# Performance work log

Hardware: AMD Instinct MI355X
Metric: run time of the kernel (lower is better)

Reference implementation:

```python
import jax, jax.numpy as jnp
import numpy as np

H = 51  # hidden size hardcoded in the module

def _lstm_cell(x, h, c, W_ih, W_hh, b_ih, b_hh):
    # PyTorch LSTMCell: gates ordered (i, f, g, o)
    z = x @ W_ih.T + h @ W_hh.T + b_ih + b_hh  # [B, 4H]
    i, f, g, o = jnp.split(z, 4, axis=-1)
    i = jax.nn.sigmoid(i)
    f = jax.nn.sigmoid(f)
    g = jnp.tanh(g)
    o = jax.nn.sigmoid(o)
    c_new = f * c + i * g
    h_new = o * jnp.tanh(c_new)
    return h_new, c_new

def setup_inputs() -> dict:
    key = jax.random.key(0)
    ks = jax.random.split(key, 12)
    B, T = 512, 512
    s = 1.0 / np.sqrt(H)  # PyTorch default init scale
    def u(k, shape):
        return jax.random.uniform(k, shape, jnp.float32, -s, s)
    return {
        "input": jax.random.normal(ks[0], (B, T), jnp.float32),
        "W_ih1": u(ks[1], (4 * H, 1)),
        "W_hh1": u(ks[2], (4 * H, H)),
        "b_ih1": u(ks[3], (4 * H,)),
        "b_hh1": u(ks[4], (4 * H,)),
        "W_ih2": u(ks[5], (4 * H, H)),
        "W_hh2": u(ks[6], (4 * H, H)),
        "b_ih2": u(ks[7], (4 * H,)),
        "b_hh2": u(ks[8], (4 * H,)),
        "W_lin": u(ks[9], (1, H)),
        "b_lin": u(ks[10], (1,)),
        "future": 0,
    }

def reference(input, W_ih1, W_hh1, b_ih1, b_hh1, W_ih2, W_hh2, b_ih2, b_hh2, W_lin, b_lin, future):
    B, T = input.shape
    h1 = jnp.zeros((B, H), input.dtype)
    c1 = jnp.zeros((B, H), input.dtype)
    h2 = jnp.zeros((B, H), input.dtype)
    c2 = jnp.zeros((B, H), input.dtype)

    def step(carry, x_t):
        h1, c1, h2, c2 = carry
        h1, c1 = _lstm_cell(x_t, h1, c1, W_ih1, W_hh1, b_ih1, b_hh1)
        h2, c2 = _lstm_cell(h1, h2, c2, W_ih2, W_hh2, b_ih2, b_hh2)
        out = h2 @ W_lin.T + b_lin  # [B, 1]
        return (h1, c1, h2, c2), out

    xs = jnp.transpose(input)[:, :, None]  # [T, B, 1]
    carry, outs = jax.lax.scan(step, (h1, c1, h2, c2), xs)
    outputs = jnp.transpose(outs[:, :, 0])  # [B, T]

    if future > 0:
        last = outs[-1]  # [B, 1]

        def fstep(carry, _):
            state, x = carry
            state, out = step(state, x)
            return (state, out), out

        _, fouts = jax.lax.scan(fstep, (carry, last), None, length=future)
        outputs = jnp.concatenate([outputs, jnp.transpose(fouts[:, :, 0])], axis=1)
    return outputs
```

## Files before the change

### kernel.cpp

```cpp
#include <hip/hip_runtime.h>

#define Hh 51
#define TT 512
#define MR 2
#define NBLK 256
#define BT 512
#define SHR 80
#define NIT 514
#define LOG2E 1.4426950408889634f

typedef _Float16 half8 __attribute__((ext_vector_type(8)));
typedef __attribute__((ext_vector_type(4))) float f32x4;

__device__ __forceinline__ float fexp2(float x){ return __builtin_amdgcn_exp2f(x); }
__device__ __forceinline__ float frcp(float x){ return __builtin_amdgcn_rcpf(x); }
__device__ __forceinline__ float sigm(float x){ return frcp(1.f + fexp2(-LOG2E*x)); }
__device__ __forceinline__ float ftanh(float x){ return 1.f - 2.f*frcp(1.f + fexp2(2.f*LOG2E*x)); }

#define MFMAH(a,b,c) __builtin_amdgcn_mfma_f32_16x16x32_f16(a,b,c,0,0,0)

__global__ __launch_bounds__(BT, 2) void lstm2_fp16u(
    const float* __restrict__ input,
    const float* __restrict__ W_ih1,
    const float* __restrict__ W_hh1,
    const float* __restrict__ b_ih1,
    const float* __restrict__ b_hh1,
    const float* __restrict__ W_ih2,
    const float* __restrict__ W_hh2,
    const float* __restrict__ b_ih2,
    const float* __restrict__ b_hh2,
    const float* __restrict__ W_lin,
    const float* __restrict__ b_lin,
    float* __restrict__ out)
{
    __shared__ float xs[TT*MR];
    __shared__ float ob[TT*MR];
    __shared__ __align__(16) _Float16 H1[2][16*SHR];
    __shared__ __align__(16) _Float16 H2[2][16*SHR];

    const int tid  = threadIdx.x;
    const int wv   = tid >> 6;
    const int lane = tid & 63;
    const int quad = lane >> 4;
    const int n16  = lane & 15;
    const int row0 = blockIdx.x * MR;
    const bool g1  = (wv < 4);
    const int  w   = g1 ? wv : (wv - 4);
    const int  l   = 13 * w + n16;
    const bool valid = (n16 <= 12) && (l < Hh);
    const bool liveA = ((n16 & 11) == 0);
    const bool updL  = (quad < MR) && valid;
    const int  fo    = n16 * SHR + quad * 8;
    const int  ho    = (quad * 4) * SHR + l;

#pragma unroll
    for (int i = 0; i < MR; ++i) {
        int idx = i * BT + tid; int m = idx >> 9, t = idx & 511;
        xs[t * MR + m] = input[(row0 + m) * TT + t];
    }
    for (int i = tid; i < 2 * 16 * SHR / 2; i += BT) {
        ((int*)H1)[i] = 0; ((int*)H2)[i] = 0;
    }

    half8 z8 = {0,0,0,0,0,0,0,0};
    half8 B1[4][2];
    half8 B2[4][2], B3[4][2];
    half8 Bout[2];
    float bb[4], wih[4];
#pragma unroll
    for (int gt = 0; gt < 4; ++gt) {
        int jrow = gt * Hh + l;
        bb[gt]  = valid ? (g1 ? (b_ih1[jrow] + b_hh1[jrow]) : (b_ih2[jrow] + b_hh2[jrow])) : 0.f;
        wih[gt] = (valid && g1) ? W_ih1[jrow] : 0.f;
#pragma unroll
        for (int kt = 0; kt < 2; ++kt) {
            B1[gt][kt] = z8; B2[gt][kt] = z8; B3[gt][kt] = z8;
#pragma unroll
            for (int jj = 0; jj < 8; ++jj) {
                int k = kt * 32 + quad * 8 + jj;
                if (valid && k < Hh) {
                    if (g1) {
                        B1[gt][kt][jj] = (_Float16)W_hh1[jrow * Hh + k];
                    } else {
                        B2[gt][kt][jj] = (_Float16)W_ih2[jrow * Hh + k];
                        B3[gt][kt][jj] = (_Float16)W_hh2[jrow * Hh + k];
                    }
                }
            }
        }
    }
#pragma unroll
    for (int kt = 0; kt < 2; ++kt) {
        Bout[kt] = z8;
#pragma unroll
        for (int jj = 0; jj < 8; ++jj) {
            int k = kt * 32 + quad * 8 + jj;
            if (wv == 7 && n16 == 0 && k < Hh)
                Bout[kt][jj] = (_Float16)W_lin[k];
        }
    }
    const float blin = b_lin[0];
    float cst = 0.f;

    half8 f1a = z8, f1b = z8;
    half8 f2a = z8, f2b = z8;

    __syncthreads();

    auto stepfn = [&](int n, int pA, int pB) {
        if (g1) {
            if (n < TT) {
                float x = xs[n * MR + quad];
                if (liveA) {
                    const _Float16* bp = &H1[pA][fo];
                    f1a = *(const half8*)(bp);
                    f1b = *(const half8*)(bp + 32);
                }
                f32x4 ac[4];
#pragma unroll
                for (int gt = 0; gt < 4; ++gt) {
                    f32x4 a = (f32x4){0.f,0.f,0.f,0.f};
                    a = MFMAH(f1a, B1[gt][0], a);
                    a = MFMAH(f1b, B1[gt][1], a);
                    ac[gt] = a;
                }
                if (updL) {
                    float zi = ac[0][0] + bb[0] + x * wih[0];
                    float zf = ac[1][0] + bb[1] + x * wih[1];
                    float zg = ac[2][0] + bb[2] + x * wih[2];
                    float zo = ac[3][0] + bb[3] + x * wih[3];
                    float ii = sigm(zi), ff = sigm(zf), gg = ftanh(zg), oo = sigm(zo);
                    cst = fmaf(ff, cst, ii * gg);
                    float h = oo * ftanh(cst);
                    H1[pB][ho] = (_Float16)h;
                }
            }
        } else if (n >= 1) {
            if (liveA) {
                f1a = *(const half8*)&H1[pA][fo];
                f1b = *(const half8*)&H1[pA][fo + 32];
                f2a = *(const half8*)&H2[pB][fo];
                f2b = *(const half8*)&H2[pB][fo + 32];
            }
            if (n <= TT) {
                f32x4 ac[4];
#pragma unroll
                for (int gt = 0; gt < 4; ++gt) {
                    f32x4 a = (f32x4){0.f,0.f,0.f,0.f};
                    a = MFMAH(f2a, B3[gt][0], a);
                    a = MFMAH(f2b, B3[gt][1], a);
                    a = MFMAH(f1a, B2[gt][0], a);
                    a = MFMAH(f1b, B2[gt][1], a);
                    ac[gt] = a;
                }
                if (updL) {
                    float zi = ac[0][0] + bb[0];
                    float zf = ac[1][0] + bb[1];
                    float zg = ac[2][0] + bb[2];
                    float zo = ac[3][0] + bb[3];
                    float ii = sigm(zi), ff = sigm(zf), gg = ftanh(zg), oo = sigm(zo);
                    cst = fmaf(ff, cst, ii * gg);
                    float h = oo * ftanh(cst);
                    H2[pA][ho] = (_Float16)h;
                }
            }
            if (wv == 7 && n >= 2) {
                f32x4 ao = (f32x4){0.f,0.f,0.f,0.f};
                ao = MFMAH(f2a, Bout[0], ao);
                ao = MFMAH(f2b, Bout[1], ao);
                if (n16 == 0 && quad < MR)
                    ob[(n - 2) * MR + quad] = ao[0] + blin;
            }
        }
        __syncthreads();
    };

    for (int k2 = 0; k2 < NIT / 2; ++k2) {
        stepfn(2 * k2,     1, 0);
        stepfn(2 * k2 + 1, 0, 1);
    }

#pragma unroll
    for (int i = 0; i < MR; ++i) {
        int idx = i * BT + tid; int m = idx >> 9, t = idx & 511;
        out[(row0 + m) * TT + t] = ob[t * MR + m];
    }
}

extern "C" void kernel_launch(void* const* d_in, const int* in_sizes, int n_in,
                              void* d_out, int out_size, void* d_ws, size_t ws_size,
                              hipStream_t stream) {
    const float* input = (const float*)d_in[0];
    const float* W_ih1 = (const float*)d_in[1];
    const float* W_hh1 = (const float*)d_in[2];
    const float* b_ih1 = (const float*)d_in[3];
    const float* b_hh1 = (const float*)d_in[4];
    const float* W_ih2 = (const float*)d_in[5];
    const float* W_hh2 = (const float*)d_in[6];
    const float* b_ih2 = (const float*)d_in[7];
    const float* b_hh2 = (const float*)d_in[8];
    const float* W_lin = (const float*)d_in[9];
    const float* b_lin = (const float*)d_in[10];
    float* out = (float*)d_out;

    hipLaunchKernelGGL(lstm2_fp16u, dim3(NBLK), dim3(BT), 0, stream,
                       input, W_ih1, W_hh1, b_ih1, b_hh1,
                       W_ih2, W_hh2, b_ih2, b_hh2, W_lin, b_lin, out);
}
```

Measured before the change: 292.9 us.

## Fold biases and input term into MFMA padding columns, move output head to wave 3

Packs the bias (as fp16 hi/lo split), the input weight and the linear-head bias into the unused K padding columns 51-54 of the weight fragments, and writes constant ones and the split-fp16 input value into the matching hidden-state columns. The gate pre-activations then come straight out of the MFMA with no scalar bias or x*w adds. The output projection moves from layer-2 wave 7 to layer-1 wave 3, which has spare MFMA capacity, shortening the layer-2 critical path. This adds extra LDS writes of x each step and relies on fp16 hi/lo splitting to keep precision.

```diff
diff --git a/kernel.cpp b/kernel.cpp
--- a/kernel.cpp
+++ b/kernel.cpp
@@ -16,10 +16,18 @@
 __device__ __forceinline__ float frcp(float x){ return __builtin_amdgcn_rcpf(x); }
 __device__ __forceinline__ float sigm(float x){ return frcp(1.f + fexp2(-LOG2E*x)); }
 __device__ __forceinline__ float ftanh(float x){ return 1.f - 2.f*frcp(1.f + fexp2(2.f*LOG2E*x)); }
+__device__ __forceinline__ unsigned short h16bits(_Float16 h){
+    union { _Float16 h; unsigned short u; } c; c.h = h; return c.u;
+}
+__device__ __forceinline__ unsigned packhl(float v){
+    _Float16 hi = (_Float16)v;
+    _Float16 lo = (_Float16)(v - (float)hi);
+    return (unsigned)h16bits(hi) | ((unsigned)h16bits(lo) << 16);
+}
 
 #define MFMAH(a,b,c) __builtin_amdgcn_mfma_f32_16x16x32_f16(a,b,c,0,0,0)
 
-__global__ __launch_bounds__(BT, 2) void lstm2_fp16u(
+__global__ __launch_bounds__(BT, 2) void lstm2_fold(
     const float* __restrict__ input,
     const float* __restrict__ W_ih1,
     const float* __restrict__ W_hh1,
@@ -33,7 +41,7 @@
     const float* __restrict__ b_lin,
     float* __restrict__ out)
 {
-    __shared__ float xs[TT*MR];
+    __shared__ unsigned xsp[(TT+1)*MR];
     __shared__ float ob[TT*MR];
     __shared__ __align__(16) _Float16 H1[2][16*SHR];
     __shared__ __align__(16) _Float16 H2[2][16*SHR];
@@ -45,19 +53,22 @@
     const int n16  = lane & 15;
     const int row0 = blockIdx.x * MR;
     const bool g1  = (wv < 4);
+    const bool w3  = (wv == 3);
     const int  w   = g1 ? wv : (wv - 4);
     const int  l   = 13 * w + n16;
     const bool valid = (n16 <= 12) && (l < Hh);
     const bool liveA = ((n16 & 11) == 0);
     const bool updL  = (quad < MR) && valid;
+    const bool xw    = (wv == 0) && (n16 == 0) && (quad < MR);
     const int  fo    = n16 * SHR + quad * 8;
     const int  ho    = (quad * 4) * SHR + l;
 
 #pragma unroll
     for (int i = 0; i < MR; ++i) {
         int idx = i * BT + tid; int m = idx >> 9, t = idx & 511;
-        xs[t * MR + m] = input[(row0 + m) * TT + t];
-    }
+        xsp[t * MR + m] = packhl(input[(row0 + m) * TT + t]);
+    }
+    if (tid < MR) xsp[TT * MR + tid] = 0u;
     for (int i = tid; i < 2 * 16 * SHR / 2; i += BT) {
         ((int*)H1)[i] = 0; ((int*)H2)[i] = 0;
     }
@@ -66,110 +77,135 @@
     half8 B1[4][2];
     half8 B2[4][2], B3[4][2];
     half8 Bout[2];
-    float bb[4], wih[4];
+    const f32x4 zc = (f32x4){0.f,0.f,0.f,0.f};
 #pragma unroll
     for (int gt = 0; gt < 4; ++gt) {
         int jrow = gt * Hh + l;
-        bb[gt]  = valid ? (g1 ? (b_ih1[jrow] + b_hh1[jrow]) : (b_ih2[jrow] + b_hh2[jrow])) : 0.f;
-        wih[gt] = (valid && g1) ? W_ih1[jrow] : 0.f;
+        float bias = 0.f, wih = 0.f;
+        if (valid) {
+            bias = g1 ? (b_ih1[jrow] + b_hh1[jrow]) : (b_ih2[jrow] + b_hh2[jrow]);
+            wih  = g1 ? W_ih1[jrow] : 0.f;
+        }
+        _Float16 bhi = (_Float16)bias;
+        _Float16 blo = (_Float16)(bias - (float)bhi);
+        _Float16 wih_h = (_Float16)wih;
 #pragma unroll
         for (int kt = 0; kt < 2; ++kt) {
             B1[gt][kt] = z8; B2[gt][kt] = z8; B3[gt][kt] = z8;
 #pragma unroll
             for (int jj = 0; jj < 8; ++jj) {
                 int k = kt * 32 + quad * 8 + jj;
-                if (valid && k < Hh) {
+                if (valid) {
                     if (g1) {
-                        B1[gt][kt][jj] = (_Float16)W_hh1[jrow * Hh + k];
+                        if (k < Hh)       B1[gt][kt][jj] = (_Float16)W_hh1[jrow * Hh + k];
+                        else if (k == 51) B1[gt][kt][jj] = bhi;
+                        else if (k == 52 || k == 53) B1[gt][kt][jj] = wih_h;
+                        else if (k == 54) B1[gt][kt][jj] = blo;
                     } else {
-                        B2[gt][kt][jj] = (_Float16)W_ih2[jrow * Hh + k];
-                        B3[gt][kt][jj] = (_Float16)W_hh2[jrow * Hh + k];
+                        if (k < Hh) {
+                            B2[gt][kt][jj] = (_Float16)W_ih2[jrow * Hh + k];
+                            B3[gt][kt][jj] = (_Float16)W_hh2[jrow * Hh + k];
+                        } else if (k == 51) B2[gt][kt][jj] = bhi;
+                        else if (k == 54)   B2[gt][kt][jj] = blo;
                     }
                 }
             }
         }
     }
-#pragma unroll
-    for (int kt = 0; kt < 2; ++kt) {
-        Bout[kt] = z8;
-#pragma unroll
-        for (int jj = 0; jj < 8; ++jj) {
-            int k = kt * 32 + quad * 8 + jj;
-            if (wv == 7 && n16 == 0 && k < Hh)
-                Bout[kt][jj] = (_Float16)W_lin[k];
-        }
-    }
-    const float blin = b_lin[0];
+    {
+        float blf = b_lin[0];
+        _Float16 blhi = (_Float16)blf;
+        _Float16 bllo = (_Float16)(blf - (float)blhi);
+#pragma unroll
+        for (int kt = 0; kt < 2; ++kt) {
+            Bout[kt] = z8;
+#pragma unroll
+            for (int jj = 0; jj < 8; ++jj) {
+                int k = kt * 32 + quad * 8 + jj;
+                if (w3 && n16 == 0) {
+                    if (k < Hh)       Bout[kt][jj] = (_Float16)W_lin[k];
+                    else if (k == 51) Bout[kt][jj] = blhi;
+                    else if (k == 54) Bout[kt][jj] = bllo;
+                }
+            }
+        }
+    }
     float cst = 0.f;
 
     half8 f1a = z8, f1b = z8;
     half8 f2a = z8, f2b = z8;
 
     __syncthreads();
+    if (tid < MR) {
+        int r = tid * 4 * SHR;
+        const unsigned one = (unsigned)h16bits((_Float16)1.0f);
+#pragma unroll
+        for (int p = 0; p < 2; ++p) {
+            H1[p][r + 51] = (_Float16)1.0f;  H1[p][r + 54] = (_Float16)1.0f;
+            H2[p][r + 51] = (_Float16)1.0f;  H2[p][r + 54] = (_Float16)1.0f;
+        }
+        *(unsigned*)&H1[1][r + 52] = xsp[tid];
+        (void)one;
+    }
+    __syncthreads();
 
     auto stepfn = [&](int n, int pA, int pB) {
         if (g1) {
+            if (w3 && n >= 2) {
+                if (liveA) {
+                    f2a = *(const half8*)&H2[pB][fo];
+                    f2b = *(const half8*)&H2[pB][fo + 32];
+                }
+            }
             if (n < TT) {
-                float x = xs[n * MR + quad];
+                unsigned xn = xw ? xsp[(n + 1) * MR + quad] : 0u;
                 if (liveA) {
-                    const _Float16* bp = &H1[pA][fo];
-                    f1a = *(const half8*)(bp);
-                    f1b = *(const half8*)(bp + 32);
+                    f1a = *(const half8*)&H1[pA][fo];
+                    f1b = *(const half8*)&H1[pA][fo + 32];
                 }
                 f32x4 ac[4];
 #pragma unroll
                 for (int gt = 0; gt < 4; ++gt) {
-                    f32x4 a = (f32x4){0.f,0.f,0.f,0.f};
-                    a = MFMAH(f1a, B1[gt][0], a);
-                    a = MFMAH(f1b, B1[gt][1], a);
+                    f32x4 a = MFMAH(f1a, B1[gt][0], zc);
+                    a       = MFMAH(f1b, B1[gt][1], a);
                     ac[gt] = a;
                 }
                 if (updL) {
-                    float zi = ac[0][0] + bb[0] + x * wih[0];
-                    float zf = ac[1][0] + bb[1] + x * wih[1];
-                    float zg = ac[2][0] + bb[2] + x * wih[2];
-                    float zo = ac[3][0] + bb[3] + x * wih[3];
-                    float ii = sigm(zi), ff = sigm(zf), gg = ftanh(zg), oo = sigm(zo);
+                    float ii = sigm(ac[0][0]), ff = sigm(ac[1][0]);
+                    float gg = ftanh(ac[2][0]), oo = sigm(ac[3][0]);
                     cst = fmaf(ff, cst, ii * gg);
                     float h = oo * ftanh(cst);
                     H1[pB][ho] = (_Float16)h;
                 }
-            }
-        } else if (n >= 1) {
+                if (xw) *(unsigned*)&H1[pB][(quad * 4) * SHR + 52] = xn;
+            }
+            if (w3 && n >= 2) {
+                f32x4 ao = MFMAH(f2a, Bout[0], zc);
+                ao       = MFMAH(f2b, Bout[1], ao);
+                if (n16 == 0 && quad < MR) ob[(n - 2) * MR + quad] = ao[0];
+            }
+        } else if (n >= 1 && n <= TT) {
             if (liveA) {
                 f1a = *(const half8*)&H1[pA][fo];
                 f1b = *(const half8*)&H1[pA][fo + 32];
                 f2a = *(const half8*)&H2[pB][fo];
                 f2b = *(const half8*)&H2[pB][fo + 32];
             }
-            if (n <= TT) {
-                f32x4 ac[4];
-#pragma unroll
-                for (int gt = 0; gt < 4; ++gt) {
-                    f32x4 a = (f32x4){0.f,0.f,0.f,0.f};
-                    a = MFMAH(f2a, B3[gt][0], a);
-                    a = MFMAH(f2b, B3[gt][1], a);
-                    a = MFMAH(f1a, B2[gt][0], a);
-                    a = MFMAH(f1b, B2[gt][1], a);
-                    ac[gt] = a;
-                }
-                if (updL) {
-                    float zi = ac[0][0] + bb[0];
-                    float zf = ac[1][0] + bb[1];
-                    float zg = ac[2][0] + bb[2];
-                    float zo = ac[3][0] + bb[3];
-                    float ii = sigm(zi), ff = sigm(zf), gg = ftanh(zg), oo = sigm(zo);
-                    cst = fmaf(ff, cst, ii * gg);
-                    float h = oo * ftanh(cst);
-                    H2[pA][ho] = (_Float16)h;
-                }
-            }
-            if (wv == 7 && n >= 2) {
-                f32x4 ao = (f32x4){0.f,0.f,0.f,0.f};
-                ao = MFMAH(f2a, Bout[0], ao);
-                ao = MFMAH(f2b, Bout[1], ao);
-                if (n16 == 0 && quad < MR)
-                    ob[(n - 2) * MR + quad] = ao[0] + blin;
+            f32x4 ac[4];
+#pragma unroll
+            for (int gt = 0; gt < 4; ++gt) {
+                f32x4 a = MFMAH(f2a, B3[gt][0], zc);
+                a       = MFMAH(f2b, B3[gt][1], a);
+                a       = MFMAH(f1a, B2[gt][0], a);
+                a       = MFMAH(f1b, B2[gt][1], a);
+                ac[gt] = a;
+            }
+            if (updL) {
+                float ii = sigm(ac[0][0]), ff = sigm(ac[1][0]);
+                float gg = ftanh(ac[2][0]), oo = sigm(ac[3][0]);
+                cst = fmaf(ff, cst, ii * gg);
+                float h = oo * ftanh(cst);
+                H2[pA][ho] = (_Float16)h;
             }
         }
         __syncthreads();
@@ -203,7 +239,7 @@
     const float* b_lin = (const float*)d_in[10];
     float* out = (float*)d_out;
 
-    hipLaunchKernelGGL(lstm2_fp16u, dim3(NBLK), dim3(BT), 0, stream,
+    hipLaunchKernelGGL(lstm2_fold, dim3(NBLK), dim3(BT), 0, stream,
                        input, W_ih1, W_hh1, b_ih1, b_hh1,
                        W_ih2, W_hh2, b_ih2, b_hh2, W_lin, b_lin, out);
 }
```

Measured after the change: 270.2 us. 1.08x faster.
